# Optimization experiments

Hardware: AMD Instinct MI355X
Metric: run time of the kernel (lower is better)

Reference implementation:

```python
import jax, jax.numpy as jnp
import numpy as np

B, S, H, NH, HD = 4, 2048, 2048, 16, 128
SCALE = HD ** -0.5


def rotate_half(x):
    x1, x2 = jnp.split(x, 2, axis=-1)
    return jnp.concatenate([-x2, x1], axis=-1)


def setup_inputs() -> dict:
    key = jax.random.key(0)
    ks = jax.random.split(key, 8)
    x = jax.random.normal(ks[0], (B, S, H), dtype=jnp.float32)
    # RoPE tables for positions 0..S-1, standard theta=10000 construction
    inv_freq = 1.0 / (10000.0 ** (jnp.arange(0, HD, 2, dtype=jnp.float32) / HD))
    t = jnp.arange(S, dtype=jnp.float32)
    freqs = jnp.einsum('s,d->sd', t, inv_freq)          # [S, HD/2]
    emb = jnp.concatenate([freqs, freqs], axis=-1)      # [S, HD]
    cos, sin = jnp.cos(emb), jnp.sin(emb)
    # causal mask: True = masked (future positions)
    mask = jnp.triu(jnp.ones((S, S), dtype=bool), k=1)
    std = H ** -0.5
    Wq = jax.random.normal(ks[1], (H, H), dtype=jnp.float32) * std
    Wk = jax.random.normal(ks[2], (H, H), dtype=jnp.float32) * std
    Wv = jax.random.normal(ks[3], (H, H), dtype=jnp.float32) * std
    Wo = jax.random.normal(ks[4], (H, H), dtype=jnp.float32) * std
    return {"x": x, "cos": cos, "sin": sin, "mask": mask,
            "Wq": Wq, "Wk": Wk, "Wv": Wv, "Wo": Wo}


def reference(x, cos, sin, mask, Wq, Wk, Wv, Wo):
    # projections: nn.Linear(bias=False) => x @ W.T
    def proj(W):
        y = jnp.einsum('bsh,ih->bsi', x, W)             # [B,S,inner]
        return y.reshape(B, S, NH, HD).transpose(0, 2, 1, 3)  # [B,NH,S,HD]
    q, k, v = proj(Wq), proj(Wk), proj(Wv)
    # RoPE (rotate-half), cos/sin broadcast over batch & heads
    c = cos[None, None, :, :]
    s = sin[None, None, :, :]
    q = q * c + rotate_half(q) * s
    k = k * c + rotate_half(k) * s
    # attention
    attn = jnp.einsum('bhqd,bhkd->bhqk', q, k) * SCALE
    attn = jnp.where(mask[None, None, :, :], -jnp.inf, attn)
    attn = jax.nn.softmax(attn, axis=-1)
    out = jnp.einsum('bhqk,bhkd->bhqd', attn, v)
    out = out.transpose(0, 2, 1, 3).reshape(B, S, NH * HD)
    y = jnp.einsum('bsi,hi->bsh', out, Wo)
    return y, k, v
```

## Files before the change

kernel.cpp:

```cpp
#include <hip/hip_runtime.h>
#include <hip/hip_bf16.h>
#include <math.h>

typedef __bf16 bf16_t;
typedef __bf16 bf16x8 __attribute__((ext_vector_type(8)));
typedef __bf16 bf16x4v __attribute__((ext_vector_type(4)));
typedef float  f32x4  __attribute__((ext_vector_type(4)));

constexpr int CB = 4, CS = 2048, CH = 2048, CNH = 16, CHD = 128;
constexpr int CM = CB * CS;
constexpr float CSCALE = 0.08838834764831845f;
constexpr float CL2E   = 1.4426950408889634f;
constexpr float CSC2   = CSCALE * CL2E;

__device__ __forceinline__ float fexp2(float x) {
  float r;
  asm("v_exp_f32 %0, %1" : "=v"(r) : "v"(x));
  return r;
}

__device__ __forceinline__ void g2l16(const void* g, void* l) {
  __builtin_amdgcn_global_load_lds(
      (const __attribute__((address_space(1))) void*)g,
      (__attribute__((address_space(3))) void*)l, 16, 0, 0);
}

__global__ __launch_bounds__(256) void cvt_kernel(const float* __restrict__ in,
                                                  bf16_t* __restrict__ out, int n4) {
  int i = blockIdx.x * 256 + threadIdx.x;
  if (i >= n4) return;
  float4 v = reinterpret_cast<const float4*>(in)[i];
  bf16x4v o = {(bf16_t)v.x, (bf16_t)v.y, (bf16_t)v.z, (bf16_t)v.w};
  reinterpret_cast<bf16x4v*>(out)[i] = o;
}

__device__ __forceinline__ void gemm256sq_core(const bf16_t* __restrict__ A,
                                               const bf16_t* __restrict__ Bm,
                                               bf16_t (*As2)[4][64 * 64],
                                               bf16_t (*Bs2)[4][64 * 64],
                                               int row0, int col0,
                                               f32x4 (&acc)[8][4]) {
  const int tid = threadIdx.x, lane = tid & 63, w = tid >> 6;
  const int wm = w >> 2, wn = w & 3;
  constexpr int NKT = CH / 64;
  const int id = w * 64 + lane;
  const int rl = id >> 3, ck = id & 7;

  auto stA = [&](int buf, int kt, int q) {
    const int row = q * 64 + rl;
    g2l16(A + (size_t)(row0 + row) * CH + kt * 64 + ((ck ^ (row & 7)) << 3),
          &As2[buf][q][id * 8]);
  };
  auto stB = [&](int buf, int kt, int q) {
    const int row = q * 64 + rl;
    g2l16(Bm + (size_t)(col0 + row) * CH + kt * 64 + ((ck ^ (row & 7)) << 3),
          &Bs2[buf][q][id * 8]);
  };
  auto rdA = [&](int buf, int r, int c) -> bf16x8 {
    return *(const bf16x8*)(&As2[buf][r >> 6][(r & 63) * 64 + ((c ^ (r & 7)) << 3)]);
  };
  auto rdB = [&](int buf, int r, int c) -> bf16x8 {
    return *(const bf16x8*)(&Bs2[buf][r >> 6][(r & 63) * 64 + ((c ^ (r & 7)) << 3)]);
  };

#pragma unroll
  for (int q = 0; q < 4; ++q) stB(0, 0, q);
#pragma unroll
  for (int q = 0; q < 4; ++q) stA(0, 0, q);
  asm volatile("s_waitcnt vmcnt(0)" ::: "memory");
  __builtin_amdgcn_s_barrier();
  __builtin_amdgcn_sched_barrier(0);

  const int ar0 = wm * 128 + (lane & 15);
  const int br0 = wn * 64 + (lane & 15);
  const int chi = lane >> 4;

  for (int t = 0; t < NKT; ++t) {
    const int buf = t & 1, nbuf = buf ^ 1;
    const bool pf = (t + 1 < NKT);
    bf16x8 bb[4][2], aa[2][2];

#pragma unroll
    for (int p = 0; p < 4; ++p) {
      if (p == 0) {
#pragma unroll
        for (int nf = 0; nf < 4; ++nf)
#pragma unroll
          for (int kk = 0; kk < 2; ++kk)
            bb[nf][kk] = rdB(buf, br0 + nf * 16, kk * 4 + chi);
      }
#pragma unroll
      for (int i = 0; i < 2; ++i)
#pragma unroll
        for (int kk = 0; kk < 2; ++kk)
          aa[i][kk] = rdA(buf, ar0 + (2 * p + i) * 16, kk * 4 + chi);

      if (pf) {
        if (p == 0) { stB(nbuf, t + 1, 0); stB(nbuf, t + 1, 1); }
        if (p == 1) { stB(nbuf, t + 1, 2); stB(nbuf, t + 1, 3); }
        if (p == 2) { stA(nbuf, t + 1, 0); stA(nbuf, t + 1, 2); }
        if (p == 3) { stA(nbuf, t + 1, 1); stA(nbuf, t + 1, 3); }
      }

      __builtin_amdgcn_s_barrier();
      asm volatile("s_waitcnt lgkmcnt(0)" ::: "memory");
      __builtin_amdgcn_sched_barrier(0);
      __builtin_amdgcn_s_setprio(1);
#pragma unroll
      for (int i = 0; i < 2; ++i)
#pragma unroll
        for (int nf = 0; nf < 4; ++nf)
#pragma unroll
          for (int kk = 0; kk < 2; ++kk)
            acc[2 * p + i][nf] = __builtin_amdgcn_mfma_f32_16x16x32_bf16(
                aa[i][kk], bb[nf][kk], acc[2 * p + i][nf], 0, 0, 0);
      __builtin_amdgcn_s_setprio(0);

      if (p == 1) {
        if (pf) { asm volatile("s_waitcnt vmcnt(4)" ::: "memory"); }
        else    { asm volatile("s_waitcnt vmcnt(0)" ::: "memory"); }
      }
      if (p == 3 && pf) { asm volatile("s_waitcnt vmcnt(2)" ::: "memory"); }
      __builtin_amdgcn_s_barrier();
      __builtin_amdgcn_sched_barrier(0);
    }
  }
}

__global__ __launch_bounds__(512, 1) void qkv_gemm(const bf16_t* __restrict__ xb,
                                                   const bf16_t* __restrict__ wqb,
                                                   const bf16_t* __restrict__ wkb,
                                                   const bf16_t* __restrict__ wvb,
                                                   bf16_t* __restrict__ qraw,
                                                   bf16_t* __restrict__ kraw,
                                                   bf16_t* __restrict__ vt,
                                                   float* __restrict__ vout) {
  __shared__ __align__(16) bf16_t As2[2][4][64 * 64];
  __shared__ __align__(16) bf16_t Bs2[2][4][64 * 64];
  const int z = blockIdx.z;
  const bf16_t* Bm = (z == 0) ? wqb : ((z == 1) ? wkb : wvb);
  const int row0 = blockIdx.x * 256, col0 = blockIdx.y * 256;
  f32x4 acc[8][4] = {};
  gemm256sq_core(xb, Bm, As2, Bs2, row0, col0, acc);

  const int lane = threadIdx.x & 63, w = threadIdx.x >> 6;
  const int wm = w >> 2, wn = w & 3;
#pragma unroll
  for (int i = 0; i < 8; ++i) {
#pragma unroll
    for (int j = 0; j < 4; ++j) {
      const int gr0 = row0 + wm * 128 + i * 16 + (lane >> 4) * 4;
      const int gc = col0 + wn * 64 + j * 16 + (lane & 15);
      const int b = gr0 >> 11, s0 = gr0 & (CS - 1);
      const int nh = gc >> 7, hd = gc & (CHD - 1);
      if (z == 2) {
#pragma unroll
        for (int r = 0; r < 4; ++r) {
          const size_t idx = ((size_t)(b * CNH + nh) * CS + s0 + r) * CHD + hd;
          vout[idx] = acc[i][j][r];
        }
        bf16x4v pv = {(bf16_t)acc[i][j][0], (bf16_t)acc[i][j][1],
                      (bf16_t)acc[i][j][2], (bf16_t)acc[i][j][3]};
        *(bf16x4v*)(vt + ((size_t)(b * CNH + nh) * CHD + hd) * CS + s0) = pv;
      } else {
        bf16_t* dst = (z == 0) ? qraw : kraw;
#pragma unroll
        for (int r = 0; r < 4; ++r) {
          const size_t idx = ((size_t)(b * CNH + nh) * CS + s0 + r) * CHD + hd;
          dst[idx] = (bf16_t)acc[i][j][r];
        }
      }
    }
  }
}

__global__ __launch_bounds__(512, 1) void y_gemm(const bf16_t* __restrict__ ob,
                                                 const bf16_t* __restrict__ wob,
                                                 float* __restrict__ yout) {
  __shared__ __align__(16) bf16_t As2[2][4][64 * 64];
  __shared__ __align__(16) bf16_t Bs2[2][4][64 * 64];
  const int row0 = blockIdx.x * 256, col0 = blockIdx.y * 256;
  f32x4 acc[8][4] = {};
  gemm256sq_core(ob, wob, As2, Bs2, row0, col0, acc);
  const int lane = threadIdx.x & 63, w = threadIdx.x >> 6;
  const int wm = w >> 2, wn = w & 3;
#pragma unroll
  for (int i = 0; i < 8; ++i)
#pragma unroll
    for (int j = 0; j < 4; ++j)
#pragma unroll
      for (int r = 0; r < 4; ++r) {
        const int gr = row0 + wm * 128 + i * 16 + (lane >> 4) * 4 + r;
        const int gc = col0 + wn * 64 + j * 16 + (lane & 15);
        yout[(size_t)gr * CH + gc] = acc[i][j][r];
      }
}

__global__ __launch_bounds__(256) void rope_kernel(bf16_t* __restrict__ qraw,
                                                   bf16_t* __restrict__ kraw,
                                                   const float* __restrict__ cosd,
                                                   const float* __restrict__ sind,
                                                   float* __restrict__ kout) {
  const int gid = blockIdx.x * 256 + threadIdx.x;
  const int isK = blockIdx.y;
  bf16_t* p = isK ? kraw : qraw;
  const int row = gid >> 3, d0 = (gid & 7) << 3;
  const int s = row & (CS - 1);
  const size_t base = (size_t)row * CHD;
  bf16x8 v1 = *(bf16x8*)(p + base + d0);
  bf16x8 v2 = *(bf16x8*)(p + base + d0 + 64);
  float c[8], sn[8];
  *(float4*)(c)      = *(const float4*)(cosd + s * CHD + d0);
  *(float4*)(c + 4)  = *(const float4*)(cosd + s * CHD + d0 + 4);
  *(float4*)(sn)     = *(const float4*)(sind + s * CHD + d0);
  *(float4*)(sn + 4) = *(const float4*)(sind + s * CHD + d0 + 4);
  float f1[8], f2[8];
  bf16x8 o1, o2;
#pragma unroll
  for (int i = 0; i < 8; ++i) {
    const float x1 = (float)v1[i], x2 = (float)v2[i];
    f1[i] = x1 * c[i] - x2 * sn[i];
    f2[i] = x2 * c[i] + x1 * sn[i];
    o1[i] = (bf16_t)f1[i];
    o2[i] = (bf16_t)f2[i];
  }
  *(bf16x8*)(p + base + d0) = o1;
  *(bf16x8*)(p + base + d0 + 64) = o2;
  if (isK) {
    *(float4*)(kout + base + d0)          = *(float4*)(f1);
    *(float4*)(kout + base + d0 + 4)      = *(float4*)(f1 + 4);
    *(float4*)(kout + base + d0 + 64)     = *(float4*)(f2);
    *(float4*)(kout + base + d0 + 64 + 4) = *(float4*)(f2 + 4);
  }
}

__global__ __launch_bounds__(256) void attn_kernel(const bf16_t* __restrict__ qb,
                                                   const bf16_t* __restrict__ kb,
                                                   const bf16_t* __restrict__ vt,
                                                   bf16_t* __restrict__ ob) {
  __shared__ __align__(16) bf16_t Ks[2][64 * 128];
  __shared__ __align__(16) bf16_t Vs[2][128 * 64];
  __shared__ __align__(16) bf16_t Ps[4][16 * 64];
  const int tid = threadIdx.x, lane = tid & 63, w = tid >> 6;

  const int swz = (blockIdx.x & 7) * 256 + (blockIdx.x >> 3);
  const int bh = swz >> 5;
  const int qt = 31 - (swz & 31);

  const int b = bh >> 4, nh = bh & (CNH - 1);
  const size_t kvbase_g = (size_t)bh * CS * CHD;
  const bf16_t* vbh = vt + (size_t)bh * CHD * CS;
  const int q0w = qt * 64 + w * 16;

  bf16x8 aq[4];
  {
    const bf16_t* qp = qb + kvbase_g + (size_t)(q0w + (lane & 15)) * CHD + (lane >> 4) * 8;
#pragma unroll
    for (int kf = 0; kf < 4; ++kf) aq[kf] = *(const bf16x8*)(qp + kf * 32);
  }

  float m_[4], l_[4];
  f32x4 o_[8];
  const f32x4 zf = {0.f, 0.f, 0.f, 0.f};
#pragma unroll
  for (int r = 0; r < 4; ++r) { m_[r] = -INFINITY; l_[r] = 0.f; }
#pragma unroll
  for (int h = 0; h < 8; ++h) o_[h] = zf;

  auto stage = [&](int buf, int kt) {
    const bf16_t* kbase = kb + kvbase_g + (size_t)kt * 64 * CHD;
#pragma unroll
    for (int i = 0; i < 4; ++i) {
      const int c = i * 256 + w * 64 + lane;
      const int r = c >> 4, ck = c & 15;
      g2l16(kbase + (size_t)r * CHD + ((ck ^ (r & 7)) << 3),
            &Ks[buf][(size_t)(i * 256 + w * 64) * 8]);
    }
#pragma unroll
    for (int i = 0; i < 4; ++i) {
      const int c = i * 256 + w * 64 + lane;
      const int r = c >> 3, ck = c & 7;
      g2l16(vbh + (size_t)r * CS + kt * 64 + ((ck ^ (r & 7)) << 3),
            &Vs[buf][(size_t)(i * 256 + w * 64) * 8]);
    }
  };

  const int nt = qt + 1;
  stage(0, 0);
  int cur = 0;

  for (int kt = 0; kt < nt; ++kt) {
    if (kt + 1 < nt) {
      stage(cur ^ 1, kt + 1);
      asm volatile("s_waitcnt vmcnt(8)" ::: "memory");
    } else {
      asm volatile("s_waitcnt vmcnt(0)" ::: "memory");
    }
    __builtin_amdgcn_s_barrier();
    __builtin_amdgcn_sched_barrier(0);

    f32x4 sf[4] = {};
#pragma unroll
    for (int kf = 0; kf < 4; ++kf) {
#pragma unroll
      for (int cf = 0; cf < 4; ++cf) {
        const int krow = cf * 16 + (lane & 15);
        const int lc = kf * 4 + (lane >> 4);
        bf16x8 bk = *(const bf16x8*)(&Ks[cur][krow * 128 + ((lc ^ (krow & 7)) << 3)]);
        sf[cf] = __builtin_amdgcn_mfma_f32_16x16x32_bf16(aq[kf], bk, sf[cf], 0, 0, 0);
      }
    }

    const int kvb = kt * 64;
    const bool diag = (kt == nt - 1);
    float tmax[4];
#pragma unroll
    for (int r = 0; r < 4; ++r) tmax[r] = -INFINITY;
#pragma unroll
    for (int cf = 0; cf < 4; ++cf) {
      const int kv = kvb + cf * 16 + (lane & 15);
#pragma unroll
      for (int r = 0; r < 4; ++r) {
        const int qr = q0w + (lane >> 4) * 4 + r;
        float xv = sf[cf][r] * CSC2;
        if (diag && kv > qr) xv = -INFINITY;
        sf[cf][r] = xv;
        tmax[r] = fmaxf(tmax[r], xv);
      }
    }
#pragma unroll
    for (int off = 1; off < 16; off <<= 1)
#pragma unroll
      for (int r = 0; r < 4; ++r)
        tmax[r] = fmaxf(tmax[r], __shfl_xor(tmax[r], off, 64));

    bool need = false;
#pragma unroll
    for (int r = 0; r < 4; ++r) need |= (tmax[r] - m_[r]) > 8.0f;
    if (__any(need)) {
#pragma unroll
      for (int r = 0; r < 4; ++r) {
        const float mn = fmaxf(m_[r], tmax[r]);
        const float corr = fexp2(m_[r] - mn);
        m_[r] = mn;
        l_[r] *= corr;
#pragma unroll
        for (int h = 0; h < 8; ++h) o_[h][r] *= corr;
      }
    }

    float psum[4] = {0.f, 0.f, 0.f, 0.f};
#pragma unroll
    for (int cf = 0; cf < 4; ++cf) {
#pragma unroll
      for (int r = 0; r < 4; ++r) {
        const float pv = fexp2(sf[cf][r] - m_[r]);
        psum[r] += pv;
        const int prow = (lane >> 4) * 4 + r;
        const int col = cf * 16 + (lane & 15);
        Ps[w][prow * 64 + (((col >> 3) ^ (prow & 7)) << 3) + (col & 7)] = (bf16_t)pv;
      }
    }
#pragma unroll
    for (int off = 1; off < 16; off <<= 1)
#pragma unroll
      for (int r = 0; r < 4; ++r)
        psum[r] += __shfl_xor(psum[r], off, 64);
#pragma unroll
    for (int r = 0; r < 4; ++r) l_[r] += psum[r];

#pragma unroll
    for (int kf = 0; kf < 2; ++kf) {
      const int prow = lane & 15;
      const int lc = kf * 4 + (lane >> 4);
      bf16x8 ap = *(const bf16x8*)(&Ps[w][prow * 64 + ((lc ^ (prow & 7)) << 3)]);
#pragma unroll
      for (int hf = 0; hf < 8; ++hf) {
        const int vrow = hf * 16 + (lane & 15);
        bf16x8 bv = *(const bf16x8*)(&Vs[cur][vrow * 64 + ((lc ^ (vrow & 7)) << 3)]);
        o_[hf] = __builtin_amdgcn_mfma_f32_16x16x32_bf16(ap, bv, o_[hf], 0, 0, 0);
      }
    }

    __builtin_amdgcn_s_barrier();
    __builtin_amdgcn_sched_barrier(0);
    cur ^= 1;
  }

#pragma unroll
  for (int r = 0; r < 4; ++r) l_[r] = 1.0f / l_[r];
  const size_t obase = (size_t)b * CS * CH;
#pragma unroll
  for (int hf = 0; hf < 8; ++hf) {
#pragma unroll
    for (int r = 0; r < 4; ++r) {
      const int qr = q0w + (lane >> 4) * 4 + r;
      const int col = nh * CHD + hf * 16 + (lane & 15);
      ob[obase + (size_t)qr * CH + col] = (bf16_t)(o_[hf][r] * l_[r]);
    }
  }
}

extern "C" void kernel_launch(void* const* d_in, const int* in_sizes, int n_in,
                              void* d_out, int out_size, void* d_ws, size_t ws_size,
                              hipStream_t stream) {
  const float* x    = (const float*)d_in[0];
  const float* cosd = (const float*)d_in[1];
  const float* sind = (const float*)d_in[2];
  const float* Wq = (const float*)d_in[4];
  const float* Wk = (const float*)d_in[5];
  const float* Wv = (const float*)d_in[6];
  const float* Wo = (const float*)d_in[7];

  float* yout = (float*)d_out;
  float* kout = yout + (size_t)CM * CH;
  float* vout = kout + (size_t)CM * CH;

  char* ws = (char*)d_ws;
  size_t off = 0;
  auto wsalloc = [&](size_t bytes) {
    void* p = ws + off;
    off += (bytes + 255) & ~(size_t)255;
    return p;
  };
  bf16_t* xb   = (bf16_t*)wsalloc((size_t)CM * CH * 2);
  bf16_t* wqb  = (bf16_t*)wsalloc((size_t)CH * CH * 2);
  bf16_t* wkb  = (bf16_t*)wsalloc((size_t)CH * CH * 2);
  bf16_t* wvb  = (bf16_t*)wsalloc((size_t)CH * CH * 2);
  bf16_t* wob  = (bf16_t*)wsalloc((size_t)CH * CH * 2);
  bf16_t* qraw = (bf16_t*)wsalloc((size_t)CM * CH * 2);
  bf16_t* kraw = (bf16_t*)wsalloc((size_t)CM * CH * 2);
  bf16_t* vt   = (bf16_t*)wsalloc((size_t)CM * CH * 2);
  bf16_t* ob   = (bf16_t*)wsalloc((size_t)CM * CH * 2);

  cvt_kernel<<<CM * CH / 4 / 256, 256, 0, stream>>>(x, xb, CM * CH / 4);
  cvt_kernel<<<CH * CH / 4 / 256, 256, 0, stream>>>(Wq, wqb, CH * CH / 4);
  cvt_kernel<<<CH * CH / 4 / 256, 256, 0, stream>>>(Wk, wkb, CH * CH / 4);
  cvt_kernel<<<CH * CH / 4 / 256, 256, 0, stream>>>(Wv, wvb, CH * CH / 4);
  cvt_kernel<<<CH * CH / 4 / 256, 256, 0, stream>>>(Wo, wob, CH * CH / 4);

  qkv_gemm<<<dim3(CM / 256, CH / 256, 3), 512, 0, stream>>>(xb, wqb, wkb, wvb,
                                                            qraw, kraw, vt, vout);
  rope_kernel<<<dim3(CB * CNH * CS * 8 / 256, 2), 256, 0, stream>>>(qraw, kraw, cosd,
                                                                    sind, kout);
  attn_kernel<<<CS / 64 * CB * CNH, 256, 0, stream>>>(qraw, kraw, vt, ob);
  y_gemm<<<dim3(CM / 256, CH / 256), 512, 0, stream>>>(ob, wob, yout);
}
```

Baseline: 552.1 us.

## Restructure attention to 32x32 MFMA transposed S^T with register-resident P

Rewrites the flash-attention kernel to compute S^T = K·Q^T using 32x32x16 MFMAs, so each lane owns a single query row. P is then packed to bf16 in registers with cvt_pk and permlane32_swap, which removes the per-wave LDS round trip for P. Query tiles grow from 64 to 128 rows per block, which halves the number of blocks and doubles K/V reuse per staged tile. Row max and row sum now need only one cross-lane shuffle, and the output is written as vector stores. The trade-offs are higher register pressure, fewer blocks for load balancing on the causal triangle, and a wider K swizzle.

```diff
diff --git a/kernel.cpp b/kernel.cpp
--- a/kernel.cpp
+++ b/kernel.cpp
@@ -6,6 +6,8 @@
 typedef __bf16 bf16x8 __attribute__((ext_vector_type(8)));
 typedef __bf16 bf16x4v __attribute__((ext_vector_type(4)));
 typedef float  f32x4  __attribute__((ext_vector_type(4)));
+typedef float  f32x16 __attribute__((ext_vector_type(16)));
+typedef unsigned int u32x4 __attribute__((ext_vector_type(4)));
 
 constexpr int CB = 4, CS = 2048, CH = 2048, CNH = 16, CHD = 128;
 constexpr int CM = CB * CS;
@@ -240,52 +242,48 @@
                                                    bf16_t* __restrict__ ob) {
   __shared__ __align__(16) bf16_t Ks[2][64 * 128];
   __shared__ __align__(16) bf16_t Vs[2][128 * 64];
-  __shared__ __align__(16) bf16_t Ps[4][16 * 64];
   const int tid = threadIdx.x, lane = tid & 63, w = tid >> 6;
-
-  const int swz = (blockIdx.x & 7) * 256 + (blockIdx.x >> 3);
-  const int bh = swz >> 5;
-  const int qt = 31 - (swz & 31);
+  const int hi = lane >> 5, l31 = lane & 31;
+
+  const int swz = (blockIdx.x & 7) * 128 + (blockIdx.x >> 3);
+  const int bh = swz >> 4;
+  const int qt = 15 - (swz & 15);
 
   const int b = bh >> 4, nh = bh & (CNH - 1);
   const size_t kvbase_g = (size_t)bh * CS * CHD;
   const bf16_t* vbh = vt + (size_t)bh * CHD * CS;
-  const int q0w = qt * 64 + w * 16;
-
-  bf16x8 aq[4];
+  const int qw0 = qt * 128 + w * 32;
+  const int qrow = qw0 + l31;
+
+  bf16x8 bq[8];
   {
-    const bf16_t* qp = qb + kvbase_g + (size_t)(q0w + (lane & 15)) * CHD + (lane >> 4) * 8;
-#pragma unroll
-    for (int kf = 0; kf < 4; ++kf) aq[kf] = *(const bf16x8*)(qp + kf * 32);
-  }
-
-  float m_[4], l_[4];
-  f32x4 o_[8];
-  const f32x4 zf = {0.f, 0.f, 0.f, 0.f};
-#pragma unroll
-  for (int r = 0; r < 4; ++r) { m_[r] = -INFINITY; l_[r] = 0.f; }
-#pragma unroll
-  for (int h = 0; h < 8; ++h) o_[h] = zf;
+    const bf16_t* qp = qb + kvbase_g + (size_t)qrow * CHD + hi * 8;
+#pragma unroll
+    for (int ks = 0; ks < 8; ++ks) bq[ks] = *(const bf16x8*)(qp + ks * 16);
+  }
+
+  float m_ = -INFINITY, l_ = 0.f;
+  f32x16 o_[4] = {};
 
   auto stage = [&](int buf, int kt) {
     const bf16_t* kbase = kb + kvbase_g + (size_t)kt * 64 * CHD;
 #pragma unroll
     for (int i = 0; i < 4; ++i) {
-      const int c = i * 256 + w * 64 + lane;
+      const int c = i * 256 + tid;
       const int r = c >> 4, ck = c & 15;
-      g2l16(kbase + (size_t)r * CHD + ((ck ^ (r & 7)) << 3),
-            &Ks[buf][(size_t)(i * 256 + w * 64) * 8]);
+      g2l16(kbase + (size_t)r * CHD + ((ck ^ (r & 15)) << 3),
+            &Ks[buf][(size_t)(i * 256 + (tid & ~63)) * 8 + (size_t)(lane) * 8]);
     }
 #pragma unroll
     for (int i = 0; i < 4; ++i) {
-      const int c = i * 256 + w * 64 + lane;
+      const int c = i * 256 + tid;
       const int r = c >> 3, ck = c & 7;
       g2l16(vbh + (size_t)r * CS + kt * 64 + ((ck ^ (r & 7)) << 3),
-            &Vs[buf][(size_t)(i * 256 + w * 64) * 8]);
-    }
-  };
-
-  const int nt = qt + 1;
+            &Vs[buf][(size_t)(i * 256 + (tid & ~63)) * 8 + (size_t)(lane) * 8]);
+    }
+  };
+
+  const int nt = 2 * qt + 2;
   stage(0, 0);
   int cur = 0;
 
@@ -299,86 +297,84 @@
     __builtin_amdgcn_s_barrier();
     __builtin_amdgcn_sched_barrier(0);
 
-    f32x4 sf[4] = {};
-#pragma unroll
-    for (int kf = 0; kf < 4; ++kf) {
-#pragma unroll
-      for (int cf = 0; cf < 4; ++cf) {
-        const int krow = cf * 16 + (lane & 15);
-        const int lc = kf * 4 + (lane >> 4);
-        bf16x8 bk = *(const bf16x8*)(&Ks[cur][krow * 128 + ((lc ^ (krow & 7)) << 3)]);
-        sf[cf] = __builtin_amdgcn_mfma_f32_16x16x32_bf16(aq[kf], bk, sf[cf], 0, 0, 0);
+    f32x16 st[2] = {};
+#pragma unroll
+    for (int kb2 = 0; kb2 < 2; ++kb2) {
+      const int krow = kb2 * 32 + l31;
+#pragma unroll
+      for (int ks = 0; ks < 8; ++ks) {
+        const int c = (ks * 2 + hi) ^ (krow & 15);
+        bf16x8 ak = *(const bf16x8*)(&Ks[cur][krow * 128 + (c << 3)]);
+        st[kb2] = __builtin_amdgcn_mfma_f32_32x32x16_bf16(ak, bq[ks], st[kb2], 0, 0, 0);
       }
     }
 
     const int kvb = kt * 64;
-    const bool diag = (kt == nt - 1);
-    float tmax[4];
-#pragma unroll
-    for (int r = 0; r < 4; ++r) tmax[r] = -INFINITY;
-#pragma unroll
-    for (int cf = 0; cf < 4; ++cf) {
-      const int kv = kvb + cf * 16 + (lane & 15);
-#pragma unroll
-      for (int r = 0; r < 4; ++r) {
-        const int qr = q0w + (lane >> 4) * 4 + r;
-        float xv = sf[cf][r] * CSC2;
-        if (diag && kv > qr) xv = -INFINITY;
-        sf[cf][r] = xv;
-        tmax[r] = fmaxf(tmax[r], xv);
-      }
-    }
-#pragma unroll
-    for (int off = 1; off < 16; off <<= 1)
-#pragma unroll
-      for (int r = 0; r < 4; ++r)
-        tmax[r] = fmaxf(tmax[r], __shfl_xor(tmax[r], off, 64));
-
-    bool need = false;
-#pragma unroll
-    for (int r = 0; r < 4; ++r) need |= (tmax[r] - m_[r]) > 8.0f;
-    if (__any(need)) {
-#pragma unroll
-      for (int r = 0; r < 4; ++r) {
-        const float mn = fmaxf(m_[r], tmax[r]);
-        const float corr = fexp2(m_[r] - mn);
-        m_[r] = mn;
-        l_[r] *= corr;
-#pragma unroll
-        for (int h = 0; h < 8; ++h) o_[h][r] *= corr;
-      }
-    }
-
-    float psum[4] = {0.f, 0.f, 0.f, 0.f};
-#pragma unroll
-    for (int cf = 0; cf < 4; ++cf) {
-#pragma unroll
-      for (int r = 0; r < 4; ++r) {
-        const float pv = fexp2(sf[cf][r] - m_[r]);
-        psum[r] += pv;
-        const int prow = (lane >> 4) * 4 + r;
-        const int col = cf * 16 + (lane & 15);
-        Ps[w][prow * 64 + (((col >> 3) ^ (prow & 7)) << 3) + (col & 7)] = (bf16_t)pv;
-      }
-    }
-#pragma unroll
-    for (int off = 1; off < 16; off <<= 1)
-#pragma unroll
-      for (int r = 0; r < 4; ++r)
-        psum[r] += __shfl_xor(psum[r], off, 64);
-#pragma unroll
-    for (int r = 0; r < 4; ++r) l_[r] += psum[r];
-
-#pragma unroll
-    for (int kf = 0; kf < 2; ++kf) {
-      const int prow = lane & 15;
-      const int lc = kf * 4 + (lane >> 4);
-      bf16x8 ap = *(const bf16x8*)(&Ps[w][prow * 64 + ((lc ^ (prow & 7)) << 3)]);
-#pragma unroll
-      for (int hf = 0; hf < 8; ++hf) {
-        const int vrow = hf * 16 + (lane & 15);
-        bf16x8 bv = *(const bf16x8*)(&Vs[cur][vrow * 64 + ((lc ^ (vrow & 7)) << 3)]);
-        o_[hf] = __builtin_amdgcn_mfma_f32_16x16x32_bf16(ap, bv, o_[hf], 0, 0, 0);
+    const bool anymask = (kvb + 63) > qw0;
+#pragma unroll
+    for (int blk = 0; blk < 2; ++blk)
+#pragma unroll
+      for (int r = 0; r < 16; ++r) {
+        float xv = st[blk][r] * CSC2;
+        if (anymask) {
+          const int kv = kvb + blk * 32 + 4 * hi + (r & 3) + 8 * (r >> 2);
+          if (kv > qrow) xv = -INFINITY;
+        }
+        st[blk][r] = xv;
+      }
+
+    float tmax = st[0][0];
+#pragma unroll
+    for (int r = 1; r < 16; ++r) tmax = fmaxf(tmax, st[0][r]);
+#pragma unroll
+    for (int r = 0; r < 16; ++r) tmax = fmaxf(tmax, st[1][r]);
+    tmax = fmaxf(tmax, __shfl_xor(tmax, 32, 64));
+
+    if (__any(tmax - m_ > 8.0f)) {
+      const float mn = fmaxf(m_, tmax);
+      const float corr = fexp2(m_ - mn);
+      m_ = mn;
+      l_ *= corr;
+#pragma unroll
+      for (int hb = 0; hb < 4; ++hb) o_[hb] *= corr;
+    }
+
+    f32x16 pe[2];
+    float psum = 0.f;
+#pragma unroll
+    for (int blk = 0; blk < 2; ++blk)
+#pragma unroll
+      for (int r = 0; r < 16; ++r) {
+        const float pv = fexp2(st[blk][r] - m_);
+        pe[blk][r] = pv;
+        psum += pv;
+      }
+    psum += __shfl_xor(psum, 32, 64);
+    l_ += psum;
+
+    bf16x8 pb[4];
+#pragma unroll
+    for (int ks = 0; ks < 4; ++ks) {
+      const int blk = ks >> 1, r0 = (ks & 1) * 8;
+      unsigned pw0, pw1, pw2, pw3;
+      asm("v_cvt_pk_bf16_f32 %0, %1, %2" : "=v"(pw0) : "v"(pe[blk][r0 + 0]), "v"(pe[blk][r0 + 1]));
+      asm("v_cvt_pk_bf16_f32 %0, %1, %2" : "=v"(pw2) : "v"(pe[blk][r0 + 4]), "v"(pe[blk][r0 + 5]));
+      asm("v_cvt_pk_bf16_f32 %0, %1, %2" : "=v"(pw1) : "v"(pe[blk][r0 + 2]), "v"(pe[blk][r0 + 3]));
+      asm("v_cvt_pk_bf16_f32 %0, %1, %2" : "=v"(pw3) : "v"(pe[blk][r0 + 6]), "v"(pe[blk][r0 + 7]));
+      asm("v_permlane32_swap_b32 %0, %1" : "+v"(pw0), "+v"(pw2));
+      asm("v_permlane32_swap_b32 %0, %1" : "+v"(pw1), "+v"(pw3));
+      u32x4 pk = {pw0, pw1, pw2, pw3};
+      pb[ks] = *reinterpret_cast<bf16x8*>(&pk);
+    }
+
+#pragma unroll
+    for (int hb = 0; hb < 4; ++hb) {
+      const int vrow = hb * 32 + l31;
+#pragma unroll
+      for (int ks = 0; ks < 4; ++ks) {
+        const int c = (ks * 2 + hi) ^ (vrow & 7);
+        bf16x8 av = *(const bf16x8*)(&Vs[cur][vrow * 64 + (c << 3)]);
+        o_[hb] = __builtin_amdgcn_mfma_f32_32x32x16_bf16(av, pb[ks], o_[hb], 0, 0, 0);
       }
     }
 
@@ -387,18 +383,16 @@
     cur ^= 1;
   }
 
-#pragma unroll
-  for (int r = 0; r < 4; ++r) l_[r] = 1.0f / l_[r];
-  const size_t obase = (size_t)b * CS * CH;
-#pragma unroll
-  for (int hf = 0; hf < 8; ++hf) {
-#pragma unroll
-    for (int r = 0; r < 4; ++r) {
-      const int qr = q0w + (lane >> 4) * 4 + r;
-      const int col = nh * CHD + hf * 16 + (lane & 15);
-      ob[obase + (size_t)qr * CH + col] = (bf16_t)(o_[hf][r] * l_[r]);
-    }
-  }
+  const float linv = 1.0f / l_;
+  bf16_t* orow = ob + ((size_t)(b * CS + qrow)) * CH + nh * CHD;
+#pragma unroll
+  for (int hb = 0; hb < 4; ++hb)
+#pragma unroll
+    for (int g = 0; g < 4; ++g) {
+      bf16x4v pv = {(bf16_t)(o_[hb][4 * g + 0] * linv), (bf16_t)(o_[hb][4 * g + 1] * linv),
+                    (bf16_t)(o_[hb][4 * g + 2] * linv), (bf16_t)(o_[hb][4 * g + 3] * linv)};
+      *(bf16x4v*)(orow + hb * 32 + 4 * hi + 8 * g) = pv;
+    }
 }
 
 extern "C" void kernel_launch(void* const* d_in, const int* in_sizes, int n_in,
@@ -443,6 +437,6 @@
                                                             qraw, kraw, vt, vout);
   rope_kernel<<<dim3(CB * CNH * CS * 8 / 256, 2), 256, 0, stream>>>(qraw, kraw, cosd,
                                                                     sind, kout);
-  attn_kernel<<<CS / 64 * CB * CNH, 256, 0, stream>>>(qraw, kraw, vt, ob);
+  attn_kernel<<<CB * CNH * (CS / 128), 256, 0, stream>>>(qraw, kraw, vt, ob);
   y_gemm<<<dim3(CM / 256, CH / 256), 512, 0, stream>>>(ob, wob, yout);
 }
```

After: 551.4 us. About the same (-0.1%).
